# Performance work log

Measured on AMD Instinct MI355X. Metric: run time of the kernel, lower is better.

The kernel has to match this reference:

```python
import jax, jax.numpy as jnp
import numpy as np

D_MODEL = 1024
NUM_HEADS = 16
D_K = D_MODEL // NUM_HEADS
SCALE = float(np.sqrt(D_K))


def setup_inputs() -> dict:
    key = jax.random.key(0)
    ks = jax.random.split(key, 12)
    B, S = 4, 2048
    s = 1.0 / np.sqrt(D_MODEL)
    inp = {
        'query': jax.random.normal(ks[0], (B, S, D_MODEL), jnp.float32),
        'key':   jax.random.normal(ks[1], (B, S, D_MODEL), jnp.float32),
        'value': jax.random.normal(ks[2], (B, S, D_MODEL), jnp.float32),
        'Wq': jax.random.normal(ks[3], (D_MODEL, D_MODEL), jnp.float32) * s,
        'bq': jax.random.normal(ks[4], (D_MODEL,), jnp.float32) * s,
        'Wk': jax.random.normal(ks[5], (D_MODEL, D_MODEL), jnp.float32) * s,
        'bk': jax.random.normal(ks[6], (D_MODEL,), jnp.float32) * s,
        'Wv': jax.random.normal(ks[7], (D_MODEL, D_MODEL), jnp.float32) * s,
        'bv': jax.random.normal(ks[8], (D_MODEL,), jnp.float32) * s,
        'Wo': jax.random.normal(ks[9], (D_MODEL, D_MODEL), jnp.float32) * s,
        'bo': jax.random.normal(ks[10], (D_MODEL,), jnp.float32) * s,
    }
    return inp


def reference(query, key, value, Wq, bq, Wk, bk, Wv, bv, Wo, bo):
    B, Sq, _ = query.shape
    Skv = key.shape[1]
    # torch Linear: x @ W.T + b
    def proj(x, W, b, S):
        y = jnp.einsum('bsd,ed->bse', x, W) + b
        return y.reshape(B, S, NUM_HEADS, D_K).transpose(0, 2, 1, 3)  # [B,H,S,dk]
    Q = proj(query, Wq, bq, Sq)
    K = proj(key, Wk, bk, Skv)
    V = proj(value, Wv, bv, Skv)
    scores = jnp.einsum('bhqd,bhkd->bhqk', Q, K) / SCALE  # [B,H,Sq,Skv]
    attn = jax.nn.softmax(scores, axis=-1)  # dropout=0 -> identity
    out = jnp.einsum('bhqk,bhkd->bhqd', attn, V)
    out = out.transpose(0, 2, 1, 3).reshape(B, Sq, D_MODEL)
    out = jnp.einsum('bsd,ed->bse', out, Wo) + bo
    return out
```

## Files before the change

kernel.cpp:

```cpp
#include <hip/hip_runtime.h>


typedef __attribute__((ext_vector_type(8))) __bf16 bf16x8;
typedef __attribute__((ext_vector_type(4))) __bf16 bf16x4;
typedef __attribute__((ext_vector_type(4))) float f32x4;
typedef __attribute__((ext_vector_type(4))) unsigned int u32x4;

#define SCALE_FOLD 0.18033688011112043f

__device__ __forceinline__ void async_copy16(const void* g, void* lds) {
  __builtin_amdgcn_global_load_lds(
      (const __attribute__((address_space(1))) void*)g,
      (__attribute__((address_space(3))) void*)lds, 16, 0, 0);
}

template <int ROWS, int THREADS>
__device__ __forceinline__ void stage_tile(const __bf16* __restrict__ g, int ld,
                                           __bf16* lds, int tid) {
  const int wave_base = tid & ~63;
#pragma unroll
  for (int r = 0; r < ROWS * 8 / THREADS; ++r) {
    int slot = r * THREADS + tid;
    int row = slot >> 3;
    int c = slot & 7;
    int gc = c ^ (row & 7);
    async_copy16(g + row * ld + gc * 8, lds + (r * THREADS + wave_base) * 8);
  }
}

__device__ __forceinline__ bf16x8 frag_ld(const __bf16* lds, int row, int chunk) {
  return *(const bf16x8*)(lds + row * 64 + ((chunk ^ (row & 7)) << 3));
}

__device__ __forceinline__ unsigned pk_bf16(float lo, float hi) {
  unsigned short l = __builtin_bit_cast(unsigned short, (__bf16)lo);
  unsigned short h = __builtin_bit_cast(unsigned short, (__bf16)hi);
  return (unsigned)l | ((unsigned)h << 16);
}

__global__ void cvt_all(const float* __restrict__ s0, const float* __restrict__ s1,
                        const float* __restrict__ s2, const float* __restrict__ s3,
                        const float* __restrict__ s4, const float* __restrict__ s5,
                        const float* __restrict__ s6, __bf16* d0, __bf16* d1,
                        __bf16* d2, __bf16* d3, __bf16* d4, __bf16* d5,
                        __bf16* d6, int n4_big, int n4_small) {
  const int z = blockIdx.y;
  const float* src;
  __bf16* dst;
  int n4;
  switch (z) {
    case 0: src = s0; dst = d0; n4 = n4_big; break;
    case 1: src = s1; dst = d1; n4 = n4_big; break;
    case 2: src = s2; dst = d2; n4 = n4_big; break;
    case 3: src = s3; dst = d3; n4 = n4_small; break;
    case 4: src = s4; dst = d4; n4 = n4_small; break;
    case 5: src = s5; dst = d5; n4 = n4_small; break;
    default: src = s6; dst = d6; n4 = n4_small; break;
  }
  int i = blockIdx.x * blockDim.x + threadIdx.x;
  if (i < n4) {
    float4 v = ((const float4*)src)[i];
    bf16x4 o = {(__bf16)v.x, (__bf16)v.y, (__bf16)v.z, (__bf16)v.w};
    ((bf16x4*)dst)[i] = o;
  }
}

__device__ __forceinline__ void gemm_body(const __bf16* __restrict__ A,
                                          const __bf16* __restrict__ B,
                                          const float* __restrict__ bias,
                                          void* __restrict__ out, int K,
                                          int mode, int m0, int n0,
                                          __bf16* Alds, __bf16* Blds) {
  const int tid = threadIdx.x;
  const int lane = tid & 63;
  const int w = tid >> 6;
  const int wm = w >> 1, wn = w & 1;
  const int l15 = lane & 15, quad = lane >> 4;

  f32x4 acc[4][4] = {};

  for (int k0 = 0; k0 < K; k0 += 64) {
    stage_tile<128, 256>(A + m0 * K + k0, K, Alds, tid);
    stage_tile<128, 256>(B + n0 * K + k0, K, Blds, tid);
    __syncthreads();
#pragma unroll
    for (int kc = 0; kc < 2; ++kc) {
      bf16x8 af[4], bfr[4];
#pragma unroll
      for (int mi = 0; mi < 4; ++mi)
        af[mi] = frag_ld(Alds, wm * 64 + mi * 16 + l15, kc * 4 + quad);
#pragma unroll
      for (int ni = 0; ni < 4; ++ni)
        bfr[ni] = frag_ld(Blds, wn * 64 + ni * 16 + l15, kc * 4 + quad);
#pragma unroll
      for (int mi = 0; mi < 4; ++mi)
#pragma unroll
        for (int ni = 0; ni < 4; ++ni)
          acc[mi][ni] = __builtin_amdgcn_mfma_f32_16x16x32_bf16(
              af[mi], bfr[ni], acc[mi][ni], 0, 0, 0);
    }
    __syncthreads();
  }

#pragma unroll
  for (int mi = 0; mi < 4; ++mi) {
#pragma unroll
    for (int i = 0; i < 4; ++i) {
      int grow = m0 + wm * 64 + mi * 16 + quad * 4 + i;
#pragma unroll
      for (int ni = 0; ni < 4; ++ni) {
        int gcol = n0 + wn * 64 + ni * 16 + l15;
        float v = acc[mi][ni][i];
        if (mode == 3) {
          v += bias[gcol];
          ((float*)out)[grow * 1024 + gcol] = v;
        } else if (mode == 2) {
          v += bias[grow];
          int h = grow >> 6, dd = grow & 63;
          int b = gcol >> 11, s = gcol & 2047;
          ((__bf16*)out)[(((b * 16 + h) * 64 + dd) * 2048) + s] = (__bf16)v;
        } else {
          v += bias[gcol];
          if (mode == 0) v *= SCALE_FOLD;
          int h = gcol >> 6, dd = gcol & 63;
          int b = grow >> 11, s = grow & 2047;
          ((__bf16*)out)[(((b * 16 + h) * 2048 + s) * 64) + dd] = (__bf16)v;
        }
      }
    }
  }
}

__device__ __forceinline__ void remap_xcd(int lid, int& mblk, int& nblk) {
  int xcd = lid & 7;
  int j = lid >> 3;
  mblk = xcd * 8 + (j >> 3);
  nblk = j & 7;
}

__global__ __launch_bounds__(256) void gemm_qkv(
    const __bf16* __restrict__ xq, const __bf16* __restrict__ xk,
    const __bf16* __restrict__ xv, const __bf16* __restrict__ wq,
    const __bf16* __restrict__ wk, const __bf16* __restrict__ wv,
    const float* __restrict__ bq, const float* __restrict__ bk,
    const float* __restrict__ bv, __bf16* Qb, __bf16* Kb, __bf16* Vtb) {
  __shared__ alignas(16) __bf16 Alds[128 * 64];
  __shared__ alignas(16) __bf16 Blds[128 * 64];
  int mblk, nblk;
  remap_xcd(blockIdx.x, mblk, nblk);
  const int z = blockIdx.y;
  if (z == 0) {
    gemm_body(xq, wq, bq, Qb, 1024, 0, mblk * 128, nblk * 128, Alds, Blds);
  } else if (z == 1) {
    gemm_body(xk, wk, bk, Kb, 1024, 1, mblk * 128, nblk * 128, Alds, Blds);
  } else {
    gemm_body(wv, xv, bv, Vtb, 1024, 2, nblk * 128, mblk * 128, Alds, Blds);
  }
}

__global__ __launch_bounds__(256) void gemm_out(const __bf16* __restrict__ A,
                                                const __bf16* __restrict__ B,
                                                const float* __restrict__ bias,
                                                float* __restrict__ out) {
  __shared__ alignas(16) __bf16 Alds[128 * 64];
  __shared__ alignas(16) __bf16 Blds[128 * 64];
  int mblk, nblk;
  remap_xcd(blockIdx.x, mblk, nblk);
  gemm_body(A, B, bias, out, 1024, 3, mblk * 128, nblk * 128, Alds, Blds);
}

__global__ __launch_bounds__(256, 4) void attn_kernel(
    const __bf16* __restrict__ Qg, const __bf16* __restrict__ Kg,
    const __bf16* __restrict__ Vt, __bf16* __restrict__ AO) {
  __shared__ alignas(16) __bf16 Klds[2][64 * 64];
  __shared__ alignas(16) __bf16 Vlds[2][64 * 64];

  const int tid = threadIdx.x;
  const int lane = tid & 63;
  const int w = tid >> 6;
  const int l15 = lane & 15, quad = lane >> 4;
  const int S = 2048;

  const int bid = blockIdx.x;
  const int r = bid >> 3;
  const int bh = (bid & 7) * 8 + (r & 7);
  const int q0 = (r >> 3) * 128;

  const __bf16* Qbase = Qg + (size_t)bh * S * 64;
  const __bf16* Kbase = Kg + (size_t)bh * S * 64;
  const __bf16* Vbase = Vt + (size_t)bh * 64 * S;

  stage_tile<128, 256>(Qbase + q0 * 64, 64, (__bf16*)Klds, tid);
  __syncthreads();
  bf16x8 qf[2][2];
#pragma unroll
  for (int qi = 0; qi < 2; ++qi)
#pragma unroll
    for (int kc = 0; kc < 2; ++kc)
      qf[qi][kc] =
          frag_ld((__bf16*)Klds, w * 32 + qi * 16 + l15, kc * 4 + quad);
  __syncthreads();

  stage_tile<64, 256>(Kbase, 64, Klds[0], tid);
  stage_tile<64, 256>(Vbase, S, Vlds[0], tid);
  __syncthreads();

  const u32x4 ones_u = {0x3F803F80u, 0x3F803F80u, 0x3F803F80u, 0x3F803F80u};
  const bf16x8 ones8 = __builtin_bit_cast(bf16x8, ones_u);

  f32x4 oacc[2][4] = {};
  f32x4 lacc[2] = {};

  for (int mt = 0; mt < 32; ++mt) {
    const int cur = mt & 1;
    if (mt + 1 < 32) {
      stage_tile<64, 256>(Kbase + (mt + 1) * 64 * 64, 64, Klds[cur ^ 1], tid);
      stage_tile<64, 256>(Vbase + (mt + 1) * 64, S, Vlds[cur ^ 1], tid);
    }

    f32x4 sacc[4][2] = {};
#pragma unroll
    for (int kc = 0; kc < 2; ++kc) {
      bf16x8 kf[4];
#pragma unroll
      for (int ci = 0; ci < 4; ++ci)
        kf[ci] = frag_ld(Klds[cur], ci * 16 + l15, kc * 4 + quad);
      __builtin_amdgcn_s_setprio(1);
#pragma unroll
      for (int ci = 0; ci < 4; ++ci)
#pragma unroll
        for (int qi = 0; qi < 2; ++qi)
          sacc[ci][qi] = __builtin_amdgcn_mfma_f32_16x16x32_bf16(
              kf[ci], qf[qi][kc], sacc[ci][qi], 0, 0, 0);
      __builtin_amdgcn_s_setprio(0);
    }

#pragma unroll
    for (int t = 0; t < 2; ++t) {
      bf16x8 vf[4];
#pragma unroll
      for (int ni = 0; ni < 4; ++ni)
        vf[ni] = frag_ld(Vlds[cur], ni * 16 + l15, t * 4 + quad);
#pragma unroll
      for (int qi = 0; qi < 2; ++qi) {
        float ea[4], eb[4];
#pragma unroll
        for (int i = 0; i < 4; ++i) {
          ea[i] = __builtin_amdgcn_exp2f(sacc[2 * t][qi][i]);
          eb[i] = __builtin_amdgcn_exp2f(sacc[2 * t + 1][qi][i]);
        }
        unsigned a0 = pk_bf16(ea[0], ea[1]);
        unsigned a1 = pk_bf16(ea[2], ea[3]);
        unsigned b0 = pk_bf16(eb[0], eb[1]);
        unsigned b1 = pk_bf16(eb[2], eb[3]);
        asm("v_permlane32_swap_b32 %0, %1" : "+v"(a0), "+v"(b0));
        asm("v_permlane16_swap_b32 %0, %1" : "+v"(a0), "+v"(b0));
        asm("v_permlane32_swap_b32 %0, %1" : "+v"(a1), "+v"(b1));
        asm("v_permlane16_swap_b32 %0, %1" : "+v"(a1), "+v"(b1));
        u32x4 pw = {a0, a1, b0, b1};
        bf16x8 pf = __builtin_bit_cast(bf16x8, pw);
        __builtin_amdgcn_s_setprio(1);
        lacc[qi] = __builtin_amdgcn_mfma_f32_16x16x32_bf16(pf, ones8, lacc[qi],
                                                           0, 0, 0);
#pragma unroll
        for (int ni = 0; ni < 4; ++ni)
          oacc[qi][ni] = __builtin_amdgcn_mfma_f32_16x16x32_bf16(
              pf, vf[ni], oacc[qi][ni], 0, 0, 0);
        __builtin_amdgcn_s_setprio(0);
      }
    }
    __syncthreads();
  }

  const int b = bh >> 4;
  const int hh = bh & 15;
#pragma unroll
  for (int qi = 0; qi < 2; ++qi) {
#pragma unroll
    for (int i = 0; i < 4; ++i) {
      int s = q0 + w * 32 + qi * 16 + quad * 4 + i;
      float inv_l = 1.f / lacc[qi][i];
#pragma unroll
      for (int ni = 0; ni < 4; ++ni) {
        int d = ni * 16 + l15;
        AO[((size_t)(b * 2048 + s)) * 1024 + hh * 64 + d] =
            (__bf16)(oacc[qi][ni][i] * inv_l);
      }
    }
  }
}

extern "C" void kernel_launch(void* const* d_in, const int* in_sizes, int n_in,
                              void* d_out, int out_size, void* d_ws,
                              size_t ws_size, hipStream_t stream) {
  const float* q_in = (const float*)d_in[0];
  const float* k_in = (const float*)d_in[1];
  const float* v_in = (const float*)d_in[2];
  const float* Wq = (const float*)d_in[3];
  const float* bq = (const float*)d_in[4];
  const float* Wk = (const float*)d_in[5];
  const float* bk = (const float*)d_in[6];
  const float* Wv = (const float*)d_in[7];
  const float* bv = (const float*)d_in[8];
  const float* Wo = (const float*)d_in[9];
  const float* bo = (const float*)d_in[10];

  const size_t SZ_X = (size_t)8192 * 1024 * 2;
  const size_t SZ_W = (size_t)1024 * 1024 * 2;
  char* p = (char*)d_ws;
  __bf16* xq = (__bf16*)p; p += SZ_X;
  __bf16* xk = (__bf16*)p; p += SZ_X;
  __bf16* xv = (__bf16*)p; p += SZ_X;
  __bf16* wqb = (__bf16*)p; p += SZ_W;
  __bf16* wkb = (__bf16*)p; p += SZ_W;
  __bf16* wvb = (__bf16*)p; p += SZ_W;
  __bf16* wob = (__bf16*)p; p += SZ_W;
  __bf16* Qb = (__bf16*)p; p += SZ_X;
  __bf16* Kb = (__bf16*)p; p += SZ_X;
  __bf16* Vtb = (__bf16*)p; p += SZ_X;
  __bf16* AOb = (__bf16*)p; p += SZ_X;

  const int nx4 = 8192 * 1024 / 4, nw4 = 1024 * 1024 / 4;
  cvt_all<<<dim3(nx4 / 256, 7), 256, 0, stream>>>(
      q_in, k_in, v_in, Wq, Wk, Wv, Wo, xq, xk, xv, wqb, wkb, wvb, wob, nx4,
      nw4);

  gemm_qkv<<<dim3(512, 3), 256, 0, stream>>>(xq, xk, xv, wqb, wkb, wvb, bq,
                                             bk, bv, Qb, Kb, Vtb);

  attn_kernel<<<1024, 256, 0, stream>>>(Qb, Kb, Vtb, AOb);

  gemm_out<<<512, 256, 0, stream>>>(AOb, wob, bo, (float*)d_out);
}
```

Before: 332.1 us.

## Replace QKV projection GEMM with 256x256 tile, 8-wave, pipelined async-LDS kernel

The fused QKV projection now uses a new 512-thread kernel with 256x256 output tiles, double-buffered LDS and a staged prefetch schedule. Quarter-tile pieces of A and B are async-loaded into LDS while MFMAs run on the current pieces, with s_setprio around the math and fine-grained vmcnt waits. The aim is more data reuse per block and less exposed global-load latency than the simple 128x128 load-sync-compute loop. In exchange it uses 128 KB of LDS per block and only 384 blocks, and the hand-tuned wait counts make correctness depend on the exact issue order of the loads.

```diff
diff --git a/kernel.cpp b/kernel.cpp
--- a/kernel.cpp
+++ b/kernel.cpp
@@ -25,6 +25,23 @@
     int c = slot & 7;
     int gc = c ^ (row & 7);
     async_copy16(g + row * ld + gc * 8, lds + (r * THREADS + wave_base) * 8);
+  }
+}
+
+template <int SH>
+__device__ __forceinline__ void stage_piece(const __bf16* __restrict__ g,
+                                            int ld, int off, __bf16* lds,
+                                            int tid) {
+  const int wave_base = tid & ~63;
+#pragma unroll
+  for (int rnd = 0; rnd < 2; ++rnd) {
+    int slot = rnd * 512 + tid;
+    int rho = slot >> 3;
+    int c = slot & 7;
+    int gc = c ^ (rho & 7);
+    int grow = ((rho >> SH) << (SH + 1)) + off + (rho & ((1 << SH) - 1));
+    async_copy16(g + (size_t)grow * ld + gc * 8,
+                 lds + (rnd * 512 + wave_base) * 8);
   }
 }
 
@@ -65,12 +82,154 @@
   }
 }
 
+__global__ __launch_bounds__(512, 2) void gemm8_qkv(
+    const __bf16* __restrict__ xq, const __bf16* __restrict__ xk,
+    const __bf16* __restrict__ xv, const __bf16* __restrict__ wq,
+    const __bf16* __restrict__ wk, const __bf16* __restrict__ wv,
+    const float* __restrict__ bq, const float* __restrict__ bk,
+    const float* __restrict__ bv, __bf16* Qb, __bf16* Kb, __bf16* Vtb) {
+  __shared__ alignas(16) __bf16 Ab[2][256 * 64];
+  __shared__ alignas(16) __bf16 Bb[2][256 * 64];
+
+  const int tid = threadIdx.x;
+  const int lane = tid & 63;
+  const int w = tid >> 6;
+  const int wm = w >> 2, wn = w & 3;
+  const int l15 = lane & 15, quad = lane >> 4;
+  const int K = 1024, NT = 16;
+
+  const int bid = blockIdx.x;
+  const int z = blockIdx.y;
+  const int xcd = bid & 7, j = bid >> 3;
+
+  const __bf16 *A, *B;
+  const float* bias;
+  __bf16* outp;
+  int mblk, nblk;
+  if (z == 0) {
+    A = xq; B = wq; bias = bq; outp = Qb;
+    mblk = xcd * 4 + (j >> 2); nblk = j & 3;
+  } else if (z == 1) {
+    A = xk; B = wk; bias = bk; outp = Kb;
+    mblk = xcd * 4 + (j >> 2); nblk = j & 3;
+  } else {
+    A = wv; B = xv; bias = bv; outp = Vtb;
+    mblk = j & 3; nblk = xcd * 4 + (j >> 2);
+  }
+  const int m0 = mblk * 256, n0 = nblk * 256;
+  const __bf16* Ag = A + (size_t)m0 * K;
+  const __bf16* Bg = B + (size_t)n0 * K;
+
+  f32x4 acc[8][4] = {};
+
+  stage_piece<6>(Ag, K, 0, Ab[0], tid);
+  stage_piece<5>(Bg, K, 32, Bb[0] + 8192, tid);
+  stage_piece<5>(Bg, K, 0, Bb[0], tid);
+  stage_piece<6>(Ag, K, 64, Ab[0] + 8192, tid);
+  stage_piece<6>(Ag + 64, K, 0, Ab[1], tid);
+  stage_piece<5>(Bg + 64, K, 32, Bb[1] + 8192, tid);
+  asm volatile("s_waitcnt vmcnt(4)" ::: "memory");
+  __builtin_amdgcn_s_barrier();
+
+  bf16x8 af[4][2];
+
+  for (int T = 0; T < NT; T += 2) {
+#pragma unroll
+    for (int pp = 0; pp < 8; ++pp) {
+      const int ph = pp & 3;
+      const int buf = pp >> 2;
+      const int mq = ph >> 1;
+      const int nh = (ph == 1 || ph == 2);
+
+      if (ph == 0 || ph == 2) {
+#pragma unroll
+        for (int mi = 0; mi < 4; ++mi)
+#pragma unroll
+          for (int kc = 0; kc < 2; ++kc)
+            af[mi][kc] = frag_ld(Ab[buf] + mq * 8192,
+                                 wm * 64 + mi * 16 + l15, kc * 4 + quad);
+      }
+      bf16x8 bfr[2][2];
+#pragma unroll
+      for (int ni = 0; ni < 2; ++ni)
+#pragma unroll
+        for (int kc = 0; kc < 2; ++kc)
+          bfr[ni][kc] = frag_ld(Bb[buf] + nh * 8192,
+                                wn * 32 + ni * 16 + l15, kc * 4 + quad);
+
+      if (pp == 0) {
+        stage_piece<5>(Bg + (size_t)(T + 1) * 64, K, 0, Bb[1], tid);
+      } else if (pp == 1) {
+        stage_piece<6>(Ag + (size_t)(T + 1) * 64, K, 64, Ab[1] + 8192, tid);
+      } else if (pp == 2) {
+        if (T + 2 < NT)
+          stage_piece<6>(Ag + (size_t)(T + 2) * 64, K, 0, Ab[0], tid);
+      } else if (pp == 3) {
+        if (T + 2 < NT)
+          stage_piece<5>(Bg + (size_t)(T + 2) * 64, K, 32, Bb[0] + 8192, tid);
+      } else if (pp == 4) {
+        if (T + 2 < NT)
+          stage_piece<5>(Bg + (size_t)(T + 2) * 64, K, 0, Bb[0], tid);
+      } else if (pp == 5) {
+        if (T + 2 < NT)
+          stage_piece<6>(Ag + (size_t)(T + 2) * 64, K, 64, Ab[0] + 8192, tid);
+      } else if (pp == 6) {
+        if (T + 3 < NT)
+          stage_piece<6>(Ag + (size_t)(T + 3) * 64, K, 0, Ab[1], tid);
+      } else {
+        if (T + 3 < NT)
+          stage_piece<5>(Bg + (size_t)(T + 3) * 64, K, 32, Bb[1] + 8192, tid);
+      }
+
+      __builtin_amdgcn_s_setprio(1);
+#pragma unroll
+      for (int kc = 0; kc < 2; ++kc)
+#pragma unroll
+        for (int mi = 0; mi < 4; ++mi)
+#pragma unroll
+          for (int ni = 0; ni < 2; ++ni)
+            acc[mq * 4 + mi][nh * 2 + ni] =
+                __builtin_amdgcn_mfma_f32_16x16x32_bf16(
+                    af[mi][kc], bfr[ni][kc], acc[mq * 4 + mi][nh * 2 + ni], 0,
+                    0, 0);
+      __builtin_amdgcn_s_setprio(0);
+      asm volatile("s_waitcnt lgkmcnt(0) vmcnt(6)" ::: "memory");
+      __builtin_amdgcn_s_barrier();
+    }
+  }
+
+#pragma unroll
+  for (int mi = 0; mi < 8; ++mi) {
+#pragma unroll
+    for (int ii = 0; ii < 4; ++ii) {
+      int grow = m0 + wm * 128 + mi * 16 + quad * 4 + ii;
+#pragma unroll
+      for (int nj = 0; nj < 4; ++nj) {
+        int gcol = n0 + wn * 64 + nj * 16 + l15;
+        float v = acc[mi][nj][ii];
+        if (z == 2) {
+          v += bias[grow];
+          int h = grow >> 6, dd = grow & 63;
+          int b = gcol >> 11, s = gcol & 2047;
+          outp[(((b * 16 + h) * 64 + dd) * 2048) + s] = (__bf16)v;
+        } else {
+          v += bias[gcol];
+          if (z == 0) v *= SCALE_FOLD;
+          int h = gcol >> 6, dd = gcol & 63;
+          int b = grow >> 11, s = grow & 2047;
+          outp[(((b * 16 + h) * 2048 + s) * 64) + dd] = (__bf16)v;
+        }
+      }
+    }
+  }
+}
+
 __device__ __forceinline__ void gemm_body(const __bf16* __restrict__ A,
                                           const __bf16* __restrict__ B,
                                           const float* __restrict__ bias,
-                                          void* __restrict__ out, int K,
-                                          int mode, int m0, int n0,
-                                          __bf16* Alds, __bf16* Blds) {
+                                          float* __restrict__ out, int K,
+                                          int m0, int n0, __bf16* Alds,
+                                          __bf16* Blds) {
   const int tid = threadIdx.x;
   const int lane = tid & 63;
   const int w = tid >> 6;
@@ -110,22 +269,7 @@
 #pragma unroll
       for (int ni = 0; ni < 4; ++ni) {
         int gcol = n0 + wn * 64 + ni * 16 + l15;
-        float v = acc[mi][ni][i];
-        if (mode == 3) {
-          v += bias[gcol];
-          ((float*)out)[grow * 1024 + gcol] = v;
-        } else if (mode == 2) {
-          v += bias[grow];
-          int h = grow >> 6, dd = grow & 63;
-          int b = gcol >> 11, s = gcol & 2047;
-          ((__bf16*)out)[(((b * 16 + h) * 64 + dd) * 2048) + s] = (__bf16)v;
-        } else {
-          v += bias[gcol];
-          if (mode == 0) v *= SCALE_FOLD;
-          int h = gcol >> 6, dd = gcol & 63;
-          int b = grow >> 11, s = grow & 2047;
-          ((__bf16*)out)[(((b * 16 + h) * 2048 + s) * 64) + dd] = (__bf16)v;
-        }
+        out[grow * 1024 + gcol] = acc[mi][ni][i] + bias[gcol];
       }
     }
   }
@@ -136,26 +280,6 @@
   int j = lid >> 3;
   mblk = xcd * 8 + (j >> 3);
   nblk = j & 7;
-}
-
-__global__ __launch_bounds__(256) void gemm_qkv(
-    const __bf16* __restrict__ xq, const __bf16* __restrict__ xk,
-    const __bf16* __restrict__ xv, const __bf16* __restrict__ wq,
-    const __bf16* __restrict__ wk, const __bf16* __restrict__ wv,
-    const float* __restrict__ bq, const float* __restrict__ bk,
-    const float* __restrict__ bv, __bf16* Qb, __bf16* Kb, __bf16* Vtb) {
-  __shared__ alignas(16) __bf16 Alds[128 * 64];
-  __shared__ alignas(16) __bf16 Blds[128 * 64];
-  int mblk, nblk;
-  remap_xcd(blockIdx.x, mblk, nblk);
-  const int z = blockIdx.y;
-  if (z == 0) {
-    gemm_body(xq, wq, bq, Qb, 1024, 0, mblk * 128, nblk * 128, Alds, Blds);
-  } else if (z == 1) {
-    gemm_body(xk, wk, bk, Kb, 1024, 1, mblk * 128, nblk * 128, Alds, Blds);
-  } else {
-    gemm_body(wv, xv, bv, Vtb, 1024, 2, nblk * 128, mblk * 128, Alds, Blds);
-  }
 }
 
 __global__ __launch_bounds__(256) void gemm_out(const __bf16* __restrict__ A,
@@ -166,7 +290,7 @@
   __shared__ alignas(16) __bf16 Blds[128 * 64];
   int mblk, nblk;
   remap_xcd(blockIdx.x, mblk, nblk);
-  gemm_body(A, B, bias, out, 1024, 3, mblk * 128, nblk * 128, Alds, Blds);
+  gemm_body(A, B, bias, out, 1024, mblk * 128, nblk * 128, Alds, Blds);
 }
 
 __global__ __launch_bounds__(256, 4) void attn_kernel(
@@ -325,8 +449,8 @@
       q_in, k_in, v_in, Wq, Wk, Wv, Wo, xq, xk, xv, wqb, wkb, wvb, wob, nx4,
       nw4);
 
-  gemm_qkv<<<dim3(512, 3), 256, 0, stream>>>(xq, xk, xv, wqb, wkb, wvb, bq,
-                                             bk, bv, Qb, Kb, Vtb);
+  gemm8_qkv<<<dim3(128, 3), 512, 0, stream>>>(xq, xk, xv, wqb, wkb, wvb, bq,
+                                              bk, bv, Qb, Kb, Vtb);
 
   attn_kernel<<<1024, 256, 0, stream>>>(Qb, Kb, Vtb, AOb);
 
```

Result: slower. 357.1 us (+7.5%).
